# Kernel tuning notes

Measured on AMD Instinct MI355X. Metric: run time of the kernel, lower is better.

Reference implementation:

```python
import jax, jax.numpy as jnp
import numpy as np

EMBED_DIM = 1024
NUM_HEADS = 16
HEAD_DIM = EMBED_DIM // NUM_HEADS
B, S = 2, 2048


def setup_inputs() -> dict:
    key = jax.random.key(0)
    ks = jax.random.split(key, 9)
    d = EMBED_DIM
    scale = 1.0 / np.sqrt(d)
    inp = {
        "x": jax.random.normal(ks[0], (B, S, d), dtype=jnp.float32),
        "mask": jnp.ones((B, S), dtype=jnp.int32),
        "Wq": jax.random.normal(ks[1], (d, d), dtype=jnp.float32) * scale,
        "bq": jnp.zeros((d,), dtype=jnp.float32),
        "Wk": jax.random.normal(ks[2], (d, d), dtype=jnp.float32) * scale,
        "bk": jnp.zeros((d,), dtype=jnp.float32),
        "Wv": jax.random.normal(ks[3], (d, d), dtype=jnp.float32) * scale,
        "bv": jnp.zeros((d,), dtype=jnp.float32),
        "Wo": jax.random.normal(ks[4], (d, d), dtype=jnp.float32) * scale,
        "bo": jnp.zeros((d,), dtype=jnp.float32),
    }
    return inp


def reference(x, mask, Wq, bq, Wk, bk, Wv, bv, Wo, bo):
    b, s, _ = x.shape
    # projections; torch Linear computes x @ W.T + b
    q = (x @ Wq.T + bq).reshape(b, s, NUM_HEADS, HEAD_DIM).transpose(0, 2, 1, 3)
    k = (x @ Wk.T + bk).reshape(b, s, NUM_HEADS, HEAD_DIM).transpose(0, 2, 1, 3)
    v = (x @ Wv.T + bv).reshape(b, s, NUM_HEADS, HEAD_DIM).transpose(0, 2, 1, 3)
    scores = jnp.einsum("bhqd,bhkd->bhqk", q, k) / np.sqrt(HEAD_DIM)  # (B,H,S,S)
    m = (mask == 0)[:, None, None, :]  # broadcast over heads and query pos
    scores = jnp.where(m, jnp.float32(-1e9), scores)
    attn = jax.nn.softmax(scores, axis=-1)
    out = jnp.einsum("bhqk,bhkd->bhqd", attn, v)
    out = out.transpose(0, 2, 1, 3).reshape(b, s, EMBED_DIM)
    return out @ Wo.T + bo
```

## Files before the change

### kernel.cpp

```cpp
#include <hip/hip_runtime.h>

#define EMBED 1024
#define NHEAD 16
#define HDIM  64
#define BB    2
#define SS    2048

typedef __bf16 bf16x8 __attribute__((ext_vector_type(8)));
typedef float  f32x4  __attribute__((ext_vector_type(4)));
typedef _Float16 f16x4 __attribute__((ext_vector_type(4)));
typedef __fp16 hf16x2 __attribute__((ext_vector_type(2)));

#if defined(__has_builtin)
#if __has_builtin(__builtin_amdgcn_exp2f)
#define EXP2(x) __builtin_amdgcn_exp2f(x)
#else
#define EXP2(x) exp2f(x)
#endif
#else
#define EXP2(x) exp2f(x)
#endif

__device__ __forceinline__ unsigned short f2bf(float f) {
  union { float f; unsigned u; } v; v.f = f;
  unsigned r = v.u + 0x7fffu + ((v.u >> 16) & 1u);
  return (unsigned short)(r >> 16);
}

__device__ __forceinline__ float bf2f(unsigned short u) {
  union { unsigned u; float f; } v; v.u = ((unsigned)u) << 16;
  return v.f;
}

__device__ __forceinline__ unsigned short f2h(float f) {
  union { _Float16 h; unsigned short u; } t;
  t.h = (_Float16)f;
  return t.u;
}

__device__ __forceinline__ void g2l16(const unsigned short* g, unsigned short* l) {
  __builtin_amdgcn_global_load_lds(
      (const __attribute__((address_space(1))) unsigned int*)g,
      (__attribute__((address_space(3))) unsigned int*)l, 16, 0, 0);
}

__global__ __launch_bounds__(256)
void cvt5_kernel(const float* __restrict__ x,  const float* __restrict__ Wq,
                 const float* __restrict__ Wk, const float* __restrict__ Wv,
                 const float* __restrict__ Wo, const int* __restrict__ mask,
                 unsigned short* __restrict__ xb,  unsigned short* __restrict__ Wqb,
                 unsigned short* __restrict__ Wkb, unsigned short* __restrict__ Wvb,
                 unsigned short* __restrict__ Wob, float* __restrict__ mbias) {
  const int i = blockIdx.x * 256 + threadIdx.x;
  if (i < (1 << 21)) {
    const float* src;
    unsigned short* dst;
    int j;
    if (i < (1 << 20)) {
      src = x; dst = xb; j = i;
    } else {
      const int t = i - (1 << 20);
      const int r = t >> 18;
      j = t & ((1 << 18) - 1);
      src = (r == 0) ? Wq : (r == 1) ? Wk : (r == 2) ? Wv : Wo;
      dst = (r == 0) ? Wqb : (r == 1) ? Wkb : (r == 2) ? Wvb : Wob;
    }
    const float4 f = ((const float4*)src)[j];
    ushort4 u;
    u.x = f2bf(f.x); u.y = f2bf(f.y); u.z = f2bf(f.z); u.w = f2bf(f.w);
    ((ushort4*)dst)[j] = u;
  } else {
    const int j = i - (1 << 21);
    const int4 m = ((const int4*)mask)[j];
    float4 o;
    o.x = m.x ? 0.f : -1e30f; o.y = m.y ? 0.f : -1e30f;
    o.z = m.z ? 0.f : -1e30f; o.w = m.w ? 0.f : -1e30f;
    ((float4*)mbias)[j] = o;
  }
}

template <typename EpiFn>
__device__ __forceinline__
void gemm_core(const unsigned short* __restrict__ A,
               const unsigned short* __restrict__ Bm,
               int m0, int n0, EpiFn epi) {
  __shared__ unsigned short sA[128 * 64];
  __shared__ unsigned short sB[128 * 64];
  const int tid = threadIdx.x;
  const int l  = tid & 63;
  const int w  = tid >> 6;
  const int lm = l & 15;
  const int qd = l >> 4;
  const int wm = w & 1;
  const int wn = w >> 1;

  f32x4 acc[4][4];
#pragma unroll
  for (int i = 0; i < 4; ++i)
#pragma unroll
    for (int j = 0; j < 4; ++j) acc[i][j] = (f32x4){0.f, 0.f, 0.f, 0.f};

  for (int k0 = 0; k0 < EMBED; k0 += 64) {
#pragma unroll
    for (int i = 0; i < 4; ++i) {
      const int t = i * 256 + tid;
      const int r = t >> 3;
      const int c = (t & 7) ^ (r & 7);
      g2l16(A + (m0 + r) * EMBED + k0 + c * 8, &sA[(i * 256 + (w << 6)) * 8]);
      g2l16(Bm + (n0 + r) * EMBED + k0 + c * 8, &sB[(i * 256 + (w << 6)) * 8]);
    }
    __syncthreads();
#pragma unroll
    for (int kk = 0; kk < 2; ++kk) {
      bf16x8 af[4], bfr[4];
#pragma unroll
      for (int mi = 0; mi < 4; ++mi) {
        const int R = wm * 64 + mi * 16 + lm;
        const int ch = R * 8 + (((kk << 2) + qd) ^ (R & 7));
        af[mi] = *(const bf16x8*)&sA[ch * 8];
      }
#pragma unroll
      for (int ni = 0; ni < 4; ++ni) {
        const int R = wn * 64 + ni * 16 + lm;
        const int ch = R * 8 + (((kk << 2) + qd) ^ (R & 7));
        bfr[ni] = *(const bf16x8*)&sB[ch * 8];
      }
#pragma unroll
      for (int mi = 0; mi < 4; ++mi)
#pragma unroll
        for (int ni = 0; ni < 4; ++ni)
          acc[mi][ni] = __builtin_amdgcn_mfma_f32_16x16x32_bf16(
              af[mi], bfr[ni], acc[mi][ni], 0, 0, 0);
    }
    __syncthreads();
  }

#pragma unroll
  for (int mi = 0; mi < 4; ++mi)
#pragma unroll
    for (int ni = 0; ni < 4; ++ni) {
      const int mb = m0 + wm * 64 + mi * 16 + qd * 4;
      const int n  = n0 + wn * 64 + ni * 16 + lm;
      epi(acc[mi][ni], mb, n);
    }
}

__device__ __forceinline__ void decode_tile(int flat, int& a0, int& b0) {
  const int sub = flat & 15;
  const int g = flat >> 4;
  a0 = ((g >> 2) * 2 + (sub >> 3));
  b0 = ((g & 3) * 8 + (sub & 7));
}

__global__ __launch_bounds__(256)
void gemm_qkv(const unsigned short* __restrict__ xb,
              const unsigned short* __restrict__ Wqb,
              const unsigned short* __restrict__ Wkb,
              const unsigned short* __restrict__ Wvb,
              const float* __restrict__ bq, const float* __restrict__ bk,
              const float* __restrict__ bv,
              unsigned short* __restrict__ Qb, unsigned short* __restrict__ Kb,
              unsigned short* __restrict__ VTb) {
  const int z = blockIdx.y;
  int a0, b0;
  decode_tile(blockIdx.x, a0, b0);
  if (z < 2) {
    const unsigned short* A = z ? Wkb : Wqb;
    const float* bias = z ? bk : bq;
    unsigned short* O = z ? Kb : Qb;
    const float scale = z ? 1.0f : 0.125f * 1.4426950408889634f;
    gemm_core(A, xb, a0 * 128, b0 * 128, [&](const f32x4& v, int mb, int n) {
      const float4 bvv = *(const float4*)&bias[mb];
      const int h = mb >> 6, d0 = mb & 63;
      const int b = n >> 11, s = n & 2047;
      ushort4 u;
      u.x = f2bf((v.x + bvv.x) * scale); u.y = f2bf((v.y + bvv.y) * scale);
      u.z = f2bf((v.z + bvv.z) * scale); u.w = f2bf((v.w + bvv.w) * scale);
      *(ushort4*)&O[(((b * NHEAD + h) * SS) + s) * HDIM + d0] = u;
    });
  } else {
    gemm_core(xb, Wvb, b0 * 128, a0 * 128, [&](const f32x4& v, int mb, int n) {
      const float bvv = bv[n];
      const int b = mb >> 11, s = mb & 2047;
      const int h = n >> 6, d = n & 63;
      ushort4 u;
      u.x = f2h(v.x + bvv); u.y = f2h(v.y + bvv);
      u.z = f2h(v.z + bvv); u.w = f2h(v.w + bvv);
      *(ushort4*)&VTb[(((b * NHEAD + h) * HDIM) + d) * SS + s] = u;
    });
  }
}

__global__ __launch_bounds__(256)
void gemm_out(const unsigned short* __restrict__ Wob,
              const unsigned short* __restrict__ Ob,
              const float* __restrict__ bo, float* __restrict__ out) {
  int a0, b0;
  decode_tile(blockIdx.x, a0, b0);
  gemm_core(Wob, Ob, a0 * 128, b0 * 128, [&](const f32x4& v, int mb, int n) {
    const float4 bvv = *(const float4*)&bo[mb];
    float4 o;
    o.x = v.x + bvv.x; o.y = v.y + bvv.y; o.z = v.z + bvv.z; o.w = v.w + bvv.w;
    *(float4*)&out[n * EMBED + mb] = o;
  });
}

__global__ __launch_bounds__(256)
void attn_kernel(const unsigned short* __restrict__ Q,
                 const unsigned short* __restrict__ K,
                 const unsigned short* __restrict__ VT,
                 const float* __restrict__ mbias,
                 unsigned short* __restrict__ Opart,
                 float* __restrict__ Lpart) {
  __shared__ unsigned short sK[64 * 64];
  __shared__ unsigned short sV[64 * 64];
  const int tid = threadIdx.x;
  const int l = tid & 63, w = tid >> 6;
  const int lm = l & 15, qd = l >> 4;
  const int b = blockIdx.z & 1, sp = blockIdx.z >> 1, h = blockIdx.y;
  const int q0 = blockIdx.x * 128 + w * 32;
  const unsigned short* Qh = Q + ((b * NHEAD + h) * SS) * HDIM;
  const unsigned short* Kh = K + ((b * NHEAD + h) * SS) * HDIM;
  const unsigned short* Vh = VT + ((b * NHEAD + h) * HDIM) * SS;
  const float* mb = mbias + b * SS;
  unsigned short* Op = Opart + sp * (BB * SS * EMBED);
  float* Lp = Lpart + sp * (BB * NHEAD * SS);

  bf16x8 qf[2][2];
#pragma unroll
  for (int g = 0; g < 2; ++g) {
    qf[g][0] = *(const bf16x8*)&Qh[(q0 + g * 16 + lm) * HDIM + qd * 8];
    qf[g][1] = *(const bf16x8*)&Qh[(q0 + g * 16 + lm) * HDIM + 32 + qd * 8];
  }

  f32x4 Od[2][4];
#pragma unroll
  for (int g = 0; g < 2; ++g)
#pragma unroll
    for (int i = 0; i < 4; ++i) Od[g][i] = (f32x4){0.f, 0.f, 0.f, 0.f};
  float lsum[2] = {0.f, 0.f};

  const int kend = sp * (SS / 2) + (SS / 2);
  for (int kb = sp * (SS / 2); kb < kend; kb += 64) {
#pragma unroll
    for (int i = 0; i < 2; ++i) {
      const int t = i * 256 + tid;
      const int r = t >> 3;
      const int c = (t & 7) ^ (r & 7);
      g2l16(Kh + (kb + r) * HDIM + c * 8, &sK[(i * 256 + (w << 6)) * 8]);
      g2l16(Vh + r * SS + kb + c * 8, &sV[(i * 256 + (w << 6)) * 8]);
    }
    __syncthreads();

    f16x4 pf[2][4];
#pragma unroll
    for (int j = 0; j < 4; ++j) {
      const int R = j * 16 + lm;
      const bf16x8 k0 = *(const bf16x8*)&sK[(R * 8 + (qd ^ (lm & 7))) * 8];
      const bf16x8 k1 = *(const bf16x8*)&sK[(R * 8 + ((4 + qd) ^ (lm & 7))) * 8];
      const float4 bj = *(const float4*)&mb[kb + j * 16 + qd * 4];
      const f32x4 binit = (f32x4){bj.x, bj.y, bj.z, bj.w};
#pragma unroll
      for (int g = 0; g < 2; ++g) {
        f32x4 t0 = binit;
        t0 = __builtin_amdgcn_mfma_f32_16x16x32_bf16(k0, qf[g][0], t0, 0, 0, 0);
        t0 = __builtin_amdgcn_mfma_f32_16x16x32_bf16(k1, qf[g][1], t0, 0, 0, 0);
        const float p0 = EXP2(t0[0]);
        const float p1 = EXP2(t0[1]);
        const float p2 = EXP2(t0[2]);
        const float p3 = EXP2(t0[3]);
        lsum[g] += (p0 + p1) + (p2 + p3);
        union { hf16x2 v[2]; f16x4 f; } pk;
        pk.v[0] = __builtin_amdgcn_cvt_pkrtz(p0, p1);
        pk.v[1] = __builtin_amdgcn_cvt_pkrtz(p2, p3);
        pf[g][j] = pk.f;
      }
    }

#pragma unroll
    for (int dt = 0; dt < 4; ++dt) {
      const int row = dt * 16 + lm;
#pragma unroll
      for (int j = 0; j < 4; ++j) {
        const int ch = (j * 2 + (qd >> 1)) ^ (lm & 7);
        const f16x4 vf = *(const f16x4*)&sV[row * 64 + ch * 8 + (qd & 1) * 4];
#pragma unroll
        for (int g = 0; g < 2; ++g)
          Od[g][dt] = __builtin_amdgcn_mfma_f32_16x16x16f16(vf, pf[g][j],
                                                            Od[g][dt], 0, 0, 0);
      }
    }
    __syncthreads();
  }

#pragma unroll
  for (int g = 0; g < 2; ++g) {
    float ls = lsum[g];
    ls += __shfl_xor(ls, 16);
    ls += __shfl_xor(ls, 32);
    if (qd == 0) Lp[(b * NHEAD + h) * SS + q0 + g * 16 + lm] = ls;
#pragma unroll
    for (int dt = 0; dt < 4; ++dt) {
      ushort4 u;
      u.x = f2bf(Od[g][dt][0]); u.y = f2bf(Od[g][dt][1]);
      u.z = f2bf(Od[g][dt][2]); u.w = f2bf(Od[g][dt][3]);
      *(ushort4*)&Op[(b * SS + q0 + g * 16 + lm) * EMBED + h * HDIM +
                     dt * 16 + qd * 4] = u;
    }
  }
}

__global__ __launch_bounds__(256)
void combine_kernel(const unsigned short* __restrict__ Opart,
                    const float* __restrict__ Lpart,
                    unsigned short* __restrict__ Ob) {
  const int i = blockIdx.x * 256 + threadIdx.x;
  const int base = i * 8;
  const int token = base >> 10;
  const int h = (base >> 6) & 15;
  const int b = token >> 11, q = token & 2047;
  const int lidx = (b * NHEAD + h) * SS + q;
  const float ls = Lpart[lidx] + Lpart[BB * NHEAD * SS + lidx];
  const float rinv = 1.f / ls;
  const ushort4* p0 = (const ushort4*)&Opart[base];
  const ushort4* p1 = (const ushort4*)&Opart[BB * SS * EMBED + base];
  ushort4 o[2];
#pragma unroll
  for (int k = 0; k < 2; ++k) {
    const ushort4 a = p0[k], c = p1[k];
    o[k].x = f2bf((bf2f(a.x) + bf2f(c.x)) * rinv);
    o[k].y = f2bf((bf2f(a.y) + bf2f(c.y)) * rinv);
    o[k].z = f2bf((bf2f(a.z) + bf2f(c.z)) * rinv);
    o[k].w = f2bf((bf2f(a.w) + bf2f(c.w)) * rinv);
  }
  *(ushort4*)&Ob[base] = o[0];
  *(ushort4*)&Ob[base + 4] = o[1];
}

extern "C" void kernel_launch(void* const* d_in, const int* in_sizes, int n_in,
                              void* d_out, int out_size, void* d_ws, size_t ws_size,
                              hipStream_t stream) {
  const float* x  = (const float*)d_in[0];
  const int* mask = (const int*)d_in[1];
  const float* Wq = (const float*)d_in[2];
  const float* bq = (const float*)d_in[3];
  const float* Wk = (const float*)d_in[4];
  const float* bk = (const float*)d_in[5];
  const float* Wv = (const float*)d_in[6];
  const float* bv = (const float*)d_in[7];
  const float* Wo = (const float*)d_in[8];
  const float* bo = (const float*)d_in[9];
  float* out = (float*)d_out;

  char* ws = (char*)d_ws;
  const size_t MB = 1024 * 1024;
  unsigned short* xb  = (unsigned short*)(ws);
  unsigned short* Ob  = (unsigned short*)(ws);
  unsigned short* Wqb = (unsigned short*)(ws + 8 * MB);
  unsigned short* Wkb = Wqb + 1024 * 1024;
  unsigned short* Wvb = Wkb + 1024 * 1024;
  unsigned short* Wob = Wvb + 1024 * 1024;
  unsigned short* Qb  = (unsigned short*)(ws + 16 * MB);
  unsigned short* Kb  = (unsigned short*)(ws + 24 * MB);
  unsigned short* VTb = (unsigned short*)(ws + 32 * MB);
  unsigned short* Opart = (unsigned short*)(ws + 40 * MB);
  float* mbb   = (float*)(ws + 56 * MB);
  float* Lpart = (float*)(ws + 56 * MB + 64 * 1024);

  cvt5_kernel<<<8196, 256, 0, stream>>>(x, Wq, Wk, Wv, Wo, mask,
                                        xb, Wqb, Wkb, Wvb, Wob, mbb);
  gemm_qkv<<<dim3(256, 3), 256, 0, stream>>>(xb, Wqb, Wkb, Wvb, bq, bk, bv,
                                             Qb, Kb, VTb);
  attn_kernel<<<dim3(16, 16, 4), 256, 0, stream>>>(Qb, Kb, VTb, mbb,
                                                   Opart, Lpart);
  combine_kernel<<<2048, 256, 0, stream>>>(Opart, Lpart, Ob);
  gemm_out<<<256, 256, 0, stream>>>(Wob, Ob, bo, out);
}
```

Measured before the change: 219.5 us.

## Double-buffer K/V tiles, stage mask in LDS, use 16x16x32 f16 MFMA for PV

New measurement: 215.9 us. About the same (-1.6%).

```diff
diff --git a/kernel.cpp b/kernel.cpp
--- a/kernel.cpp
+++ b/kernel.cpp
@@ -8,7 +8,7 @@
 
 typedef __bf16 bf16x8 __attribute__((ext_vector_type(8)));
 typedef float  f32x4  __attribute__((ext_vector_type(4)));
-typedef _Float16 f16x4 __attribute__((ext_vector_type(4)));
+typedef _Float16 f16x8 __attribute__((ext_vector_type(8)));
 typedef __fp16 hf16x2 __attribute__((ext_vector_type(2)));
 
 #if defined(__has_builtin)
@@ -173,10 +173,13 @@
       const float4 bvv = *(const float4*)&bias[mb];
       const int h = mb >> 6, d0 = mb & 63;
       const int b = n >> 11, s = n & 2047;
+      int sw = s;
+      if (z == 1)
+        sw = (s & ~31) | (((s >> 2) & 1) << 4) | (((s >> 3) & 3) << 2) | (s & 3);
       ushort4 u;
       u.x = f2bf((v.x + bvv.x) * scale); u.y = f2bf((v.y + bvv.y) * scale);
       u.z = f2bf((v.z + bvv.z) * scale); u.w = f2bf((v.w + bvv.w) * scale);
-      *(ushort4*)&O[(((b * NHEAD + h) * SS) + s) * HDIM + d0] = u;
+      *(ushort4*)&O[(((b * NHEAD + h) * SS) + sw) * HDIM + d0] = u;
     });
   } else {
     gemm_core(xb, Wvb, b0 * 128, a0 * 128, [&](const f32x4& v, int mb, int n) {
@@ -212,8 +215,9 @@
                  const float* __restrict__ mbias,
                  unsigned short* __restrict__ Opart,
                  float* __restrict__ Lpart) {
-  __shared__ unsigned short sK[64 * 64];
-  __shared__ unsigned short sV[64 * 64];
+  __shared__ unsigned short sK[2][64 * 64];
+  __shared__ unsigned short sV[2][64 * 64];
+  __shared__ float sMB[SS / 2];
   const int tid = threadIdx.x;
   const int l = tid & 63, w = tid >> 6;
   const int lm = l & 15, qd = l >> 4;
@@ -222,9 +226,10 @@
   const unsigned short* Qh = Q + ((b * NHEAD + h) * SS) * HDIM;
   const unsigned short* Kh = K + ((b * NHEAD + h) * SS) * HDIM;
   const unsigned short* Vh = VT + ((b * NHEAD + h) * HDIM) * SS;
-  const float* mb = mbias + b * SS;
+  const float* mb = mbias + b * SS + sp * (SS / 2);
   unsigned short* Op = Opart + sp * (BB * SS * EMBED);
   float* Lp = Lpart + sp * (BB * NHEAD * SS);
+  const int kb0 = sp * (SS / 2);
 
   bf16x8 qf[2][2];
 #pragma unroll
@@ -233,61 +238,77 @@
     qf[g][1] = *(const bf16x8*)&Qh[(q0 + g * 16 + lm) * HDIM + 32 + qd * 8];
   }
 
-  f32x4 Od[2][4];
-#pragma unroll
-  for (int g = 0; g < 2; ++g)
-#pragma unroll
-    for (int i = 0; i < 4; ++i) Od[g][i] = (f32x4){0.f, 0.f, 0.f, 0.f};
-  float lsum[2] = {0.f, 0.f};
-
-  const int kend = sp * (SS / 2) + (SS / 2);
-  for (int kb = sp * (SS / 2); kb < kend; kb += 64) {
+  auto stageKV = [&](int buf, int kb) {
 #pragma unroll
     for (int i = 0; i < 2; ++i) {
       const int t = i * 256 + tid;
       const int r = t >> 3;
       const int c = (t & 7) ^ (r & 7);
-      g2l16(Kh + (kb + r) * HDIM + c * 8, &sK[(i * 256 + (w << 6)) * 8]);
-      g2l16(Vh + r * SS + kb + c * 8, &sV[(i * 256 + (w << 6)) * 8]);
-    }
-    __syncthreads();
-
-    f16x4 pf[2][4];
-#pragma unroll
-    for (int j = 0; j < 4; ++j) {
-      const int R = j * 16 + lm;
-      const bf16x8 k0 = *(const bf16x8*)&sK[(R * 8 + (qd ^ (lm & 7))) * 8];
-      const bf16x8 k1 = *(const bf16x8*)&sK[(R * 8 + ((4 + qd) ^ (lm & 7))) * 8];
-      const float4 bj = *(const float4*)&mb[kb + j * 16 + qd * 4];
-      const f32x4 binit = (f32x4){bj.x, bj.y, bj.z, bj.w};
-#pragma unroll
-      for (int g = 0; g < 2; ++g) {
-        f32x4 t0 = binit;
-        t0 = __builtin_amdgcn_mfma_f32_16x16x32_bf16(k0, qf[g][0], t0, 0, 0, 0);
-        t0 = __builtin_amdgcn_mfma_f32_16x16x32_bf16(k1, qf[g][1], t0, 0, 0, 0);
-        const float p0 = EXP2(t0[0]);
-        const float p1 = EXP2(t0[1]);
-        const float p2 = EXP2(t0[2]);
-        const float p3 = EXP2(t0[3]);
-        lsum[g] += (p0 + p1) + (p2 + p3);
-        union { hf16x2 v[2]; f16x4 f; } pk;
-        pk.v[0] = __builtin_amdgcn_cvt_pkrtz(p0, p1);
-        pk.v[1] = __builtin_amdgcn_cvt_pkrtz(p2, p3);
-        pf[g][j] = pk.f;
+      g2l16(Kh + (kb + r) * HDIM + c * 8, &sK[buf][(i * 256 + (w << 6)) * 8]);
+      g2l16(Vh + r * SS + kb + c * 8, &sV[buf][(i * 256 + (w << 6)) * 8]);
+    }
+  };
+
+  g2l16((const unsigned short*)(mb + tid * 4), (unsigned short*)&sMB[w * 256]);
+  stageKV(0, kb0);
+
+  f32x4 Od[2][4];
+#pragma unroll
+  for (int g = 0; g < 2; ++g)
+#pragma unroll
+    for (int i = 0; i < 4; ++i) Od[g][i] = (f32x4){0.f, 0.f, 0.f, 0.f};
+  float lsum[2] = {0.f, 0.f};
+
+  __syncthreads();
+
+  const int NT = (SS / 2) / 64;
+  for (int t = 0; t < NT; ++t) {
+    const int curb = t & 1;
+    if (t + 1 < NT) stageKV(curb ^ 1, kb0 + (t + 1) * 64);
+
+    f16x8 pf8[2][2];
+#pragma unroll
+    for (int p = 0; p < 2; ++p) {
+      union PK { hf16x2 h2[4]; f16x8 v; } pk0, pk1;
+#pragma unroll
+      for (int jj = 0; jj < 2; ++jj) {
+        const int j = p * 2 + jj;
+        const int R = j * 16 + lm;
+        const bf16x8 k0 = *(const bf16x8*)&sK[curb][(R * 8 + (qd ^ (lm & 7))) * 8];
+        const bf16x8 k1 = *(const bf16x8*)&sK[curb][(R * 8 + ((4 + qd) ^ (lm & 7))) * 8];
+        const float4 bj = *(const float4*)&sMB[t * 64 + p * 32 + qd * 8 + jj * 4];
+        const f32x4 binit = (f32x4){bj.x, bj.y, bj.z, bj.w};
+#pragma unroll
+        for (int g = 0; g < 2; ++g) {
+          f32x4 t0 = binit;
+          t0 = __builtin_amdgcn_mfma_f32_16x16x32_bf16(k0, qf[g][0], t0, 0, 0, 0);
+          t0 = __builtin_amdgcn_mfma_f32_16x16x32_bf16(k1, qf[g][1], t0, 0, 0, 0);
+          const float p0 = EXP2(t0[0]);
+          const float p1 = EXP2(t0[1]);
+          const float p2 = EXP2(t0[2]);
+          const float p3 = EXP2(t0[3]);
+          lsum[g] += (p0 + p1) + (p2 + p3);
+          const hf16x2 lo = __builtin_amdgcn_cvt_pkrtz(p0, p1);
+          const hf16x2 hi = __builtin_amdgcn_cvt_pkrtz(p2, p3);
+          if (g == 0) { pk0.h2[jj * 2] = lo; pk0.h2[jj * 2 + 1] = hi; }
+          else        { pk1.h2[jj * 2] = lo; pk1.h2[jj * 2 + 1] = hi; }
+        }
       }
+      pf8[0][p] = pk0.v;
+      pf8[1][p] = pk1.v;
     }
 
 #pragma unroll
     for (int dt = 0; dt < 4; ++dt) {
       const int row = dt * 16 + lm;
 #pragma unroll
-      for (int j = 0; j < 4; ++j) {
-        const int ch = (j * 2 + (qd >> 1)) ^ (lm & 7);
-        const f16x4 vf = *(const f16x4*)&sV[row * 64 + ch * 8 + (qd & 1) * 4];
-#pragma unroll
-        for (int g = 0; g < 2; ++g)
-          Od[g][dt] = __builtin_amdgcn_mfma_f32_16x16x16f16(vf, pf[g][j],
-                                                            Od[g][dt], 0, 0, 0);
+      for (int p = 0; p < 2; ++p) {
+        const f16x8 vf =
+            *(const f16x8*)&sV[curb][row * 64 + ((p * 4 + qd) ^ (lm & 7)) * 8];
+        Od[0][dt] = __builtin_amdgcn_mfma_f32_16x16x32_f16(vf, pf8[0][p],
+                                                           Od[0][dt], 0, 0, 0);
+        Od[1][dt] = __builtin_amdgcn_mfma_f32_16x16x32_f16(vf, pf8[1][p],
+                                                           Od[1][dt], 0, 0, 0);
       }
     }
     __syncthreads();
```
